# Kernel optimization log

Hardware: AMD Instinct MI355X
Metric: run time of the kernel (lower is better)

The kernel has to match this reference:

```python
import jax, jax.numpy as jnp
import numpy as np
from jax import lax

B, S, L, H, D_IN, W = 128, 64, 137, 128, 64, 256  # batch, segments, logsig_dim, hidden, input_dim, vf_width


def setup_inputs() -> dict:
    key = jax.random.key(0)
    ks = jax.random.split(key, 12)
    rn = lambda k, s, sc: jax.random.normal(k, s, dtype=jnp.float32) * sc
    return {
        "times": jnp.arange(S + 1, dtype=jnp.float32),
        "logsig": rn(ks[0], (B, S, L), 0.1),
        "initial": rn(ks[1], (B, D_IN), 1.0),
        "in_w": rn(ks[2], (D_IN, H), 0.12),
        "in_b": rn(ks[3], (H,), 0.05),
        "h1_w": rn(ks[4], (H, W), 0.09),
        "h1_b": rn(ks[5], (W,), 0.05),
        "h2_w": rn(ks[6], (W, W), 0.06),
        "h2_b": rn(ks[7], (W,), 0.05),
        "vo_w": rn(ks[8], (W, W), 0.06),
        "vo_b": rn(ks[9], (W,), 0.05),
        "ml_w": rn(ks[10], (W, H * (L - 1)), 0.02),
        "ml_b": rn(ks[11], (H * (L - 1),), 0.01),
    }


def reference(times, logsig, initial, in_w, in_b, h1_w, h1_b, h2_w, h2_b, vo_w, vo_b, ml_w, ml_b):
    intervals = times                 # [S+1]; forward requires times == registered intervals
    coeffs = logsig[:, :, 1:]         # [B, S, L-1] (first logsig channel dropped)
    h0 = initial @ in_w + in_b        # [B, H]

    def func(t, y):
        # searchsorted + clamp, exactly as in the torch module
        idx = jnp.clip(jnp.searchsorted(intervals, t, side='left'), 1, S)
        dt = intervals[idx] - intervals[idx - 1]
        coeff = jnp.take(coeffs, idx - 1, axis=1)        # [B, L-1]
        h = jax.nn.relu(y @ h1_w + h1_b)                 # vf MLP (vf_depth-1 = 2 hidden layers)
        h = jax.nn.relu(h @ h2_w + h2_b)
        h = jnp.tanh(h @ vo_w + vo_b)                    # final tanh activation
        vf = (h @ ml_w + ml_b).reshape(B, H, L - 1)      # [B, H, L-1]
        return jnp.einsum('bhd,bd->bh', vf, coeff) / dt  # [B, H]

    def step(y, n):
        # one fixed-size Heun (RK2) step from intervals[n] to intervals[n+1]
        t0, t1 = intervals[n], intervals[n + 1]
        dt = t1 - t0
        k1 = func(t0, y)
        k2 = func(t1, y + dt * k1)
        y1 = y + 0.5 * dt * (k1 + k2)
        return y1, y1

    _, ys = lax.scan(step, h0, jnp.arange(S))            # ys: [S, B, H]
    features = jnp.concatenate([h0[:, None, :], jnp.swapaxes(ys, 0, 1)], axis=1)  # [B, S+1, H]
    return features, features[:, -1]
```

## Files before the change

kernel.cpp:

```cpp
#include <hip/hip_runtime.h>
#include <hip/hip_bf16.h>


#define BB 128
#define SS 64
#define LL 137
#define HH 128
#define DIN 64
#define WW 256
#define DD 136
#define KP 160
#define NC 32768
#define OUT2_OFF ((size_t)BB*(SS+1)*HH)

typedef __hip_bfloat16 bf16;
typedef __attribute__((ext_vector_type(8))) short short8;
typedef __attribute__((ext_vector_type(4))) float f32x4;
typedef _Float16 h2t __attribute__((ext_vector_type(2)));

__device__ __forceinline__ bf16 f2bf(float x){ return __float2bfloat16(x); }

__device__ __forceinline__ float fdot2u(unsigned w, unsigned y, float acc){
#if __has_builtin(__builtin_amdgcn_fdot2)
  return __builtin_amdgcn_fdot2(__builtin_bit_cast(h2t, w),
                                __builtin_bit_cast(h2t, y), acc, false);
#else
  h2t a = __builtin_bit_cast(h2t, w), b2 = __builtin_bit_cast(h2t, y);
  return acc + (float)a[0]*(float)b2[0] + (float)a[1]*(float)b2[1];
#endif
}
__device__ __forceinline__ float dot8(uint4 w, uint4 y, float acc){
  acc = fdot2u(w.x, y.x, acc);
  acc = fdot2u(w.y, y.y, acc);
  acc = fdot2u(w.z, y.z, acc);
  acc = fdot2u(w.w, y.w, acc);
  return acc;
}

__global__ void prep_coeff(const float* __restrict__ logsig, bf16* __restrict__ cA){
  int m = blockIdx.x;
  int d = threadIdx.x;
  int a = m >> 7, b = m & 127;
  float v = 0.0f;
  if (d < DD) v = logsig[(size_t)(b*SS + a)*LL + 1 + d];
  cA[(size_t)m*KP + d] = f2bf(v);
}

__global__ void prep_btt(const float* __restrict__ mlw, bf16* __restrict__ btt){
  int c = blockIdx.x;
  int d = threadIdx.x;
  int w = ((c >> 10) << 3) | (c & 7);
  int h = (c >> 3) & 127;
  float v = 0.0f;
  if (d < DD) v = mlw[(size_t)w*(HH*DD) + h*DD + d];
  btt[(size_t)c*KP + d] = f2bf(v);
}

__global__ void prep_packw(const float* __restrict__ src, uint4* __restrict__ dst){
  int c = blockIdx.x, j = threadIdx.x;
  union { _Float16 h[8]; uint4 v; } u;
  #pragma unroll
  for (int r = 0; r < 8; ++r) u.h[r] = (_Float16)src[(size_t)(c*8+r)*WW + j];
  dst[c*WW + j] = u.v;
}

__global__ void abias_kernel(const float* __restrict__ mlb, const float* __restrict__ logsig,
                             float* __restrict__ Abias){
  int a = blockIdx.x, b = blockIdx.y;
  int h = threadIdx.x;
  __shared__ float cf[DD];
  for (int d = h; d < DD; d += HH) cf[d] = logsig[(size_t)(b*SS + a)*LL + 1 + d];
  __syncthreads();
  float acc = 0.f;
  const float* mb = mlb + (size_t)h*DD;
  #pragma unroll 8
  for (int d = 0; d < DD; ++d) acc += cf[d] * mb[d];
  Abias[((size_t)a*BB + b)*HH + h] = acc;
}

#define AST 40
__global__ __launch_bounds__(256) void agemm_kernel(const bf16* __restrict__ cA,
                                                    const bf16* __restrict__ btt,
                                                    _Float16* __restrict__ As, int mAbs0){
  __shared__ __align__(16) short a_sm[64*AST];
  __shared__ __align__(16) short b_sm[128*AST];
  __shared__ __align__(16) short o_sm[64*136];
  int mt = blockIdx.x, nt = blockIdx.y;
  int t = threadIdx.x, lane = t & 63, wid = t >> 6;
  int mBlockAbs = mAbs0 + mt*64;
  int c0 = nt*128;
  int mW = (wid & 1)*32, cW = (wid >> 1)*64;

  f32x4 acc[2][4];
  for (int i = 0; i < 2; ++i)
    for (int j = 0; j < 4; ++j)
      acc[i][j] = (f32x4){0.f,0.f,0.f,0.f};

  for (int kk = 0; kk < 5; ++kk){
    int d0 = kk*32;
    {
      int row = t >> 2, seg = t & 3;
      uint4 v = *(const uint4*)(cA + (size_t)(mBlockAbs+row)*KP + d0 + seg*8);
      *(uint4*)&a_sm[row*AST + seg*8] = v;
    }
    #pragma unroll
    for (int rep = 0; rep < 2; ++rep){
      int idx = t + rep*256;
      int row = idx >> 2, seg = idx & 3;
      uint4 v = *(const uint4*)(btt + (size_t)(c0+row)*KP + d0 + seg*8);
      *(uint4*)&b_sm[row*AST + seg*8] = v;
    }
    __syncthreads();
    int mr = lane & 15, q = lane >> 4;
    short8 af[2], bfr[4];
    #pragma unroll
    for (int mi = 0; mi < 2; ++mi) af[mi]  = *(const short8*)&a_sm[(mW + mi*16 + mr)*AST + q*8];
    #pragma unroll
    for (int ci = 0; ci < 4; ++ci) bfr[ci] = *(const short8*)&b_sm[(cW + ci*16 + mr)*AST + q*8];
    #pragma unroll
    for (int mi = 0; mi < 2; ++mi)
      #pragma unroll
      for (int ci = 0; ci < 4; ++ci)
        acc[mi][ci] = __builtin_amdgcn_mfma_f32_16x16x32_bf16(af[mi], bfr[ci], acc[mi][ci], 0, 0, 0);
    __syncthreads();
  }

  {
    int mr = lane & 15, q = lane >> 4;
    #pragma unroll
    for (int mi = 0; mi < 2; ++mi)
      #pragma unroll
      for (int ci = 0; ci < 4; ++ci){
        int col = cW + ci*16 + mr;
        #pragma unroll
        for (int r = 0; r < 4; ++r){
          int row = mW + mi*16 + q*4 + r;
          _Float16 hv = (_Float16)acc[mi][ci][r];
          o_sm[row*136 + col] = *(short*)&hv;
        }
      }
  }
  __syncthreads();
  int mLocBlock = mt*64;
  #pragma unroll
  for (int rep = 0; rep < 4; ++rep){
    int idx = t + rep*256;
    int row = idx >> 4, seg = idx & 15;
    uint4 v = *(const uint4*)&o_sm[row*136 + seg*8];
    *(uint4*)(As + (size_t)(mLocBlock + row)*NC + c0 + seg*8) = v;
  }
}

__device__ __forceinline__ void nrde_func(
    int b, int wave, int lane,
    const uint4* __restrict__ wp1, const uint4* __restrict__ wp2,
    const uint4* vo_sm,
    const _Float16* yh, _Float16* h1h, _Float16* h2h, _Float16* h3h,
    const float* bs1, const float* bs2, const float* bsv,
    const _Float16* __restrict__ As, const float* __restrict__ Abias,
    int aLoc, int aAbs, float inv_dtf, float* kout)
{
  const int j = (wave << 4) | (lane & 15);
  const int q = lane >> 4;
  {
    const uint4* wp = wp1 + (q << 2)*WW + j;
    const uint4* yp = (const uint4*)yh + (q << 2);
    float acc = 0.f;
    #pragma unroll
    for (int cc = 0; cc < 4; ++cc) acc = dot8(wp[cc*WW], yp[cc], acc);
    acc += __shfl_xor(acc, 16);
    acc += __shfl_xor(acc, 32);
    if (q == 0){ float v = bs1[j] + acc; h1h[j] = (_Float16)(v > 0.f ? v : 0.f); }
  }
  __syncthreads();
  {
    const uint4* wp = wp2 + (q << 3)*WW + j;
    const uint4* hp = (const uint4*)h1h + (q << 3);
    float acc = 0.f;
    #pragma unroll
    for (int cc = 0; cc < 8; ++cc) acc = dot8(wp[cc*WW], hp[cc], acc);
    acc += __shfl_xor(acc, 16);
    acc += __shfl_xor(acc, 32);
    if (q == 0){ float v = bs2[j] + acc; h2h[j] = (_Float16)(v > 0.f ? v : 0.f); }
  }
  __syncthreads();
  {
    const uint4* wp = vo_sm + (q << 3)*WW + j;
    const uint4* hp = (const uint4*)h2h + (q << 3);
    float acc = 0.f;
    #pragma unroll
    for (int cc = 0; cc < 8; ++cc) acc = dot8(wp[cc*WW], hp[cc], acc);
    acc += __shfl_xor(acc, 16);
    acc += __shfl_xor(acc, 32);
    if (q == 0) h3h[j] = (_Float16)tanhf(bsv[j] + acc);
  }
  __syncthreads();
  {
    const int h  = (wave << 3) | (lane & 7);
    const int q8 = lane >> 3;
    const uint4* Ap = (const uint4*)(As + (size_t)(aLoc*BB + b)*NC);
    const uint4* hp = (const uint4*)h3h + (q8 << 2);
    float ab = (q8 == 0) ? Abias[((size_t)aAbs*BB + b)*HH + h] : 0.f;
    float acc = 0.f;
    #pragma unroll
    for (int cc = 0; cc < 4; ++cc)
      acc = dot8(Ap[((q8 << 2) + cc)*HH + h], hp[cc], acc);
    acc += ab;
    acc += __shfl_xor(acc, 8);
    acc += __shfl_xor(acc, 16);
    acc += __shfl_xor(acc, 32);
    if (q8 == 0) kout[h] = acc * inv_dtf;
  }
}

__global__ __launch_bounds__(1024) void scan_kernel(
    const float* __restrict__ times, const float* __restrict__ initial,
    const float* __restrict__ in_w, const float* __restrict__ in_b,
    const float* __restrict__ h1_b, const float* __restrict__ h2_b,
    const float* __restrict__ vo_b,
    const uint4* __restrict__ wp1, const uint4* __restrict__ wp2,
    const uint4* __restrict__ wpv,
    const _Float16* __restrict__ As, const float* __restrict__ Abias,
    float* __restrict__ y_state, float* __restrict__ out,
    int s0, int s1, int aBase)
{
  __shared__ __align__(16) uint4 vo_sm[32*WW];
  __shared__ __align__(16) _Float16 yh[HH];
  __shared__ __align__(16) _Float16 h1h[WW];
  __shared__ __align__(16) _Float16 h2h[WW];
  __shared__ __align__(16) _Float16 h3h[WW];
  __shared__ float yv[HH], kk1[HH], kk2[HH];
  __shared__ float bs1[WW], bs2[WW], bsv[WW];

  const int b = blockIdx.x, t = threadIdx.x;
  const int wave = t >> 6, lane = t & 63;

  for (int i = t; i < 32*WW; i += 1024) vo_sm[i] = wpv[i];
  if (t < WW){ bs1[t] = h1_b[t]; bs2[t] = h2_b[t]; bsv[t] = vo_b[t]; }

  if (s0 == 0){
    if (t < HH){
      float acc = in_b[t];
      for (int i = 0; i < DIN; ++i)
        acc += initial[b*DIN + i] * in_w[(size_t)i*HH + t];
      yv[t] = acc; yh[t] = (_Float16)acc;
      out[(size_t)b*(SS+1)*HH + t] = acc;
    }
  } else if (t < HH){
    float v = y_state[b*HH + t];
    yv[t] = v; yh[t] = (_Float16)v;
  }
  __syncthreads();

  for (int n = s0; n < s1; ++n){
    float t0v = times[n], t1v = times[n+1];
    float dt = t1v - t0v;
    int idx1 = (n >= 1) ? n : 1;
    float dtf1 = times[idx1] - times[idx1-1];
    int a1 = (n >= 1) ? (n-1) : 0;
    nrde_func(b, wave, lane, wp1, wp2, vo_sm, yh, h1h, h2h, h3h, bs1, bs2, bsv,
              As, Abias, a1 - aBase, a1, 1.f/dtf1, kk1);
    __syncthreads();
    if (t < HH) yh[t] = (_Float16)(yv[t] + dt*kk1[t]);
    __syncthreads();
    nrde_func(b, wave, lane, wp1, wp2, vo_sm, yh, h1h, h2h, h3h, bs1, bs2, bsv,
              As, Abias, n - aBase, n, 1.f/dt, kk2);
    __syncthreads();
    if (t < HH){
      float ynew = yv[t] + 0.5f*dt*(kk1[t] + kk2[t]);
      yv[t] = ynew; yh[t] = (_Float16)ynew;
      out[((size_t)b*(SS+1) + (n+1))*HH + t] = ynew;
    }
    __syncthreads();
  }

  if (t < HH){
    y_state[b*HH + t] = yv[t];
    if (s1 == SS) out[OUT2_OFF + (size_t)b*HH + t] = yv[t];
  }
}

extern "C" void kernel_launch(void* const* d_in, const int* in_sizes, int n_in,
                              void* d_out, int out_size, void* d_ws, size_t ws_size,
                              hipStream_t stream)
{
  (void)in_sizes; (void)n_in; (void)out_size;
  const float* times   = (const float*)d_in[0];
  const float* logsig  = (const float*)d_in[1];
  const float* initial = (const float*)d_in[2];
  const float* in_w    = (const float*)d_in[3];
  const float* in_b    = (const float*)d_in[4];
  const float* h1_w    = (const float*)d_in[5];
  const float* h1_b    = (const float*)d_in[6];
  const float* h2_w    = (const float*)d_in[7];
  const float* h2_b    = (const float*)d_in[8];
  const float* vo_w    = (const float*)d_in[9];
  const float* vo_b    = (const float*)d_in[10];
  const float* ml_w    = (const float*)d_in[11];
  const float* ml_b    = (const float*)d_in[12];
  float* out = (float*)d_out;

  char* ws = (char*)d_ws;
  size_t off = 0;
  bf16* cA      = (bf16*)(ws + off); off += (size_t)8192*KP*2;
  bf16* btt     = (bf16*)(ws + off); off += (size_t)NC*KP*2;
  float* Abias  = (float*)(ws + off); off += (size_t)SS*BB*HH*4;
  float* y_state= (float*)(ws + off); off += (size_t)BB*HH*4;
  uint4* wp1    = (uint4*)(ws + off); off += (size_t)16*WW*16;
  uint4* wp2    = (uint4*)(ws + off); off += (size_t)32*WW*16;
  uint4* wpv    = (uint4*)(ws + off); off += (size_t)32*WW*16;
  _Float16* As  = (_Float16*)(ws + off);
  size_t perA = (size_t)BB*HH*WW*2;
  size_t avail = (ws_size > off) ? (ws_size - off) : 0;
  int C = (int)(avail / perA);
  if (C > SS) C = SS;
  if (C < 2) return;

  prep_coeff<<<8192, 160, 0, stream>>>(logsig, cA);
  prep_btt<<<NC, 160, 0, stream>>>(ml_w, btt);
  abias_kernel<<<dim3(SS, BB), HH, 0, stream>>>(ml_b, logsig, Abias);
  prep_packw<<<16, WW, 0, stream>>>(h1_w, wp1);
  prep_packw<<<32, WW, 0, stream>>>(h2_w, wp2);
  prep_packw<<<32, WW, 0, stream>>>(vo_w, wpv);

  int s = 0, aB = 0;
  while (s < SS){
    int cc = SS - aB; if (cc > C) cc = C;
    agemm_kernel<<<dim3(cc*2, 256), 256, 0, stream>>>(cA, btt, As, aB*BB);
    int sEnd = aB + cc; if (sEnd > SS) sEnd = SS;
    scan_kernel<<<BB, 1024, 0, stream>>>(times, initial, in_w, in_b,
        h1_b, h2_b, vo_b, wp1, wp2, wpv, As, Abias, y_state, out, s, sEnd, aB);
    s = sEnd;
    aB = sEnd - 1;
  }
}
```

Measured before the change: 729.9 us.

## Preload GEMM K-slices, prefetch scan weights into registers, use fast tanh

The agemm kernel now loads all five K-slices of A and B into shared memory up front with one barrier, replacing the per-slice load/sync loop, and reuses that buffer for the output staging. In the scan's vector-field function, the global weights for layers 1 and 2 and the As/Abias operands are loaded into registers at function entry, so their latency overlaps the earlier layers instead of sitting between barriers. Dot-product chains are split into two accumulators for more ILP, and tanhf is replaced with an exp/reciprocal approximation. Register pressure rises and the fast tanh slightly changes numerics.

New measurement: 695.5 us. 1.05x faster.

```diff
diff --git a/kernel.cpp b/kernel.cpp
--- a/kernel.cpp
+++ b/kernel.cpp
@@ -37,6 +37,16 @@
   return acc;
 }
 
+__device__ __forceinline__ float fast_tanh(float x){
+  float e = __expf(2.f*x);
+#if __has_builtin(__builtin_amdgcn_rcpf)
+  float r = __builtin_amdgcn_rcpf(e + 1.f);
+#else
+  float r = 1.f/(e + 1.f);
+#endif
+  return 1.f - 2.f*r;
+}
+
 __global__ void prep_coeff(const float* __restrict__ logsig, bf16* __restrict__ cA){
   int m = blockIdx.x;
   int d = threadIdx.x;
@@ -79,74 +89,82 @@
 }
 
 #define AST 40
-__global__ __launch_bounds__(256) void agemm_kernel(const bf16* __restrict__ cA,
-                                                    const bf16* __restrict__ btt,
-                                                    _Float16* __restrict__ As, int mAbs0){
-  __shared__ __align__(16) short a_sm[64*AST];
-  __shared__ __align__(16) short b_sm[128*AST];
-  __shared__ __align__(16) short o_sm[64*136];
+#define ASM_SZ (5*64*AST)
+#define BSM_SZ (5*128*AST)
+__global__ __launch_bounds__(256, 2) void agemm_kernel(const bf16* __restrict__ cA,
+                                                       const bf16* __restrict__ btt,
+                                                       _Float16* __restrict__ As, int mAbs0){
+  __shared__ __align__(16) short sm[ASM_SZ + BSM_SZ];
+  short* a_sm = sm;
+  short* b_sm = sm + ASM_SZ;
   int mt = blockIdx.x, nt = blockIdx.y;
   int t = threadIdx.x, lane = t & 63, wid = t >> 6;
   int mBlockAbs = mAbs0 + mt*64;
   int c0 = nt*128;
   int mW = (wid & 1)*32, cW = (wid >> 1)*64;
 
+  #pragma unroll
+  for (int r = 0; r < 5; ++r){
+    int idx = t + r*256;
+    int kk = idx >> 8, rem = idx & 255;
+    int row = rem >> 2, seg = rem & 3;
+    uint4 v = *(const uint4*)(cA + (size_t)(mBlockAbs+row)*KP + kk*32 + seg*8);
+    *(uint4*)&a_sm[(kk*64 + row)*AST + seg*8] = v;
+  }
+  #pragma unroll
+  for (int r = 0; r < 10; ++r){
+    int idx = t + r*256;
+    int kk = idx >> 9, rem = idx & 511;
+    int row = rem >> 2, seg = rem & 3;
+    uint4 v = *(const uint4*)(btt + (size_t)(c0+row)*KP + kk*32 + seg*8);
+    *(uint4*)&b_sm[(kk*128 + row)*AST + seg*8] = v;
+  }
+  __syncthreads();
+
   f32x4 acc[2][4];
+  #pragma unroll
   for (int i = 0; i < 2; ++i)
+    #pragma unroll
     for (int j = 0; j < 4; ++j)
       acc[i][j] = (f32x4){0.f,0.f,0.f,0.f};
 
+  int mr = lane & 15, q = lane >> 4;
+  #pragma unroll
   for (int kk = 0; kk < 5; ++kk){
-    int d0 = kk*32;
-    {
-      int row = t >> 2, seg = t & 3;
-      uint4 v = *(const uint4*)(cA + (size_t)(mBlockAbs+row)*KP + d0 + seg*8);
-      *(uint4*)&a_sm[row*AST + seg*8] = v;
-    }
-    #pragma unroll
-    for (int rep = 0; rep < 2; ++rep){
-      int idx = t + rep*256;
-      int row = idx >> 2, seg = idx & 3;
-      uint4 v = *(const uint4*)(btt + (size_t)(c0+row)*KP + d0 + seg*8);
-      *(uint4*)&b_sm[row*AST + seg*8] = v;
-    }
-    __syncthreads();
-    int mr = lane & 15, q = lane >> 4;
     short8 af[2], bfr[4];
     #pragma unroll
-    for (int mi = 0; mi < 2; ++mi) af[mi]  = *(const short8*)&a_sm[(mW + mi*16 + mr)*AST + q*8];
-    #pragma unroll
-    for (int ci = 0; ci < 4; ++ci) bfr[ci] = *(const short8*)&b_sm[(cW + ci*16 + mr)*AST + q*8];
+    for (int mi = 0; mi < 2; ++mi)
+      af[mi]  = *(const short8*)&a_sm[(kk*64 + mW + mi*16 + mr)*AST + q*8];
+    #pragma unroll
+    for (int ci = 0; ci < 4; ++ci)
+      bfr[ci] = *(const short8*)&b_sm[(kk*128 + cW + ci*16 + mr)*AST + q*8];
     #pragma unroll
     for (int mi = 0; mi < 2; ++mi)
       #pragma unroll
       for (int ci = 0; ci < 4; ++ci)
         acc[mi][ci] = __builtin_amdgcn_mfma_f32_16x16x32_bf16(af[mi], bfr[ci], acc[mi][ci], 0, 0, 0);
-    __syncthreads();
-  }
-
-  {
-    int mr = lane & 15, q = lane >> 4;
-    #pragma unroll
-    for (int mi = 0; mi < 2; ++mi)
+  }
+  __syncthreads();
+
+  #pragma unroll
+  for (int mi = 0; mi < 2; ++mi)
+    #pragma unroll
+    for (int ci = 0; ci < 4; ++ci){
+      int col = cW + ci*16 + mr;
       #pragma unroll
-      for (int ci = 0; ci < 4; ++ci){
-        int col = cW + ci*16 + mr;
-        #pragma unroll
-        for (int r = 0; r < 4; ++r){
-          int row = mW + mi*16 + q*4 + r;
-          _Float16 hv = (_Float16)acc[mi][ci][r];
-          o_sm[row*136 + col] = *(short*)&hv;
-        }
+      for (int r = 0; r < 4; ++r){
+        int row = mW + mi*16 + q*4 + r;
+        _Float16 hv = (_Float16)acc[mi][ci][r];
+        sm[row*136 + col] = *(short*)&hv;
       }
-  }
+    }
   __syncthreads();
   int mLocBlock = mt*64;
   #pragma unroll
   for (int rep = 0; rep < 4; ++rep){
     int idx = t + rep*256;
     int row = idx >> 4, seg = idx & 15;
-    uint4 v = *(const uint4*)&o_sm[row*136 + seg*8];
+    uint4 v = *(const uint4*)&sm[row*136 + seg*8];
     *(uint4*)(As + (size_t)(mLocBlock + row)*NC + c0 + seg*8) = v;
   }
 }
@@ -160,25 +178,49 @@
     const _Float16* __restrict__ As, const float* __restrict__ Abias,
     int aLoc, int aAbs, float inv_dtf, float* kout)
 {
-  const int j = (wave << 4) | (lane & 15);
-  const int q = lane >> 4;
+  const int j  = (wave << 4) | (lane & 15);
+  const int q  = lane >> 4;
+  const int h  = (wave << 3) | (lane & 7);
+  const int q8 = lane >> 3;
+
+  uint4 w1r[4], w2r[8], ar[4];
   {
     const uint4* wp = wp1 + (q << 2)*WW + j;
+    #pragma unroll
+    for (int cc = 0; cc < 4; ++cc) w1r[cc] = wp[cc*WW];
+  }
+  {
+    const uint4* wp = wp2 + (q << 3)*WW + j;
+    #pragma unroll
+    for (int cc = 0; cc < 8; ++cc) w2r[cc] = wp[cc*WW];
+  }
+  {
+    const uint4* Ap = (const uint4*)(As + ((size_t)aLoc*BB + b)*NC);
+    #pragma unroll
+    for (int cc = 0; cc < 4; ++cc) ar[cc] = Ap[((q8 << 2) + cc)*HH + h];
+  }
+  float ab = (q8 == 0) ? Abias[((size_t)aAbs*BB + b)*HH + h] : 0.f;
+
+  {
     const uint4* yp = (const uint4*)yh + (q << 2);
-    float acc = 0.f;
-    #pragma unroll
-    for (int cc = 0; cc < 4; ++cc) acc = dot8(wp[cc*WW], yp[cc], acc);
+    float a0 = 0.f, a1 = 0.f;
+    a0 = dot8(w1r[0], yp[0], a0); a1 = dot8(w1r[1], yp[1], a1);
+    a0 = dot8(w1r[2], yp[2], a0); a1 = dot8(w1r[3], yp[3], a1);
+    float acc = a0 + a1;
     acc += __shfl_xor(acc, 16);
     acc += __shfl_xor(acc, 32);
     if (q == 0){ float v = bs1[j] + acc; h1h[j] = (_Float16)(v > 0.f ? v : 0.f); }
   }
   __syncthreads();
   {
-    const uint4* wp = wp2 + (q << 3)*WW + j;
     const uint4* hp = (const uint4*)h1h + (q << 3);
-    float acc = 0.f;
-    #pragma unroll
-    for (int cc = 0; cc < 8; ++cc) acc = dot8(wp[cc*WW], hp[cc], acc);
+    float a0 = 0.f, a1 = 0.f;
+    #pragma unroll
+    for (int cc = 0; cc < 8; cc += 2){
+      a0 = dot8(w2r[cc],   hp[cc],   a0);
+      a1 = dot8(w2r[cc+1], hp[cc+1], a1);
+    }
+    float acc = a0 + a1;
     acc += __shfl_xor(acc, 16);
     acc += __shfl_xor(acc, 32);
     if (q == 0){ float v = bs2[j] + acc; h2h[j] = (_Float16)(v > 0.f ? v : 0.f); }
@@ -187,25 +229,24 @@
   {
     const uint4* wp = vo_sm + (q << 3)*WW + j;
     const uint4* hp = (const uint4*)h2h + (q << 3);
-    float acc = 0.f;
-    #pragma unroll
-    for (int cc = 0; cc < 8; ++cc) acc = dot8(wp[cc*WW], hp[cc], acc);
+    float a0 = 0.f, a1 = 0.f;
+    #pragma unroll
+    for (int cc = 0; cc < 8; cc += 2){
+      a0 = dot8(wp[cc*WW],     hp[cc],   a0);
+      a1 = dot8(wp[(cc+1)*WW], hp[cc+1], a1);
+    }
+    float acc = a0 + a1;
     acc += __shfl_xor(acc, 16);
     acc += __shfl_xor(acc, 32);
-    if (q == 0) h3h[j] = (_Float16)tanhf(bsv[j] + acc);
-  }
-  __syncthreads();
-  {
-    const int h  = (wave << 3) | (lane & 7);
-    const int q8 = lane >> 3;
-    const uint4* Ap = (const uint4*)(As + (size_t)(aLoc*BB + b)*NC);
+    if (q == 0) h3h[j] = (_Float16)fast_tanh(bsv[j] + acc);
+  }
+  __syncthreads();
+  {
     const uint4* hp = (const uint4*)h3h + (q8 << 2);
-    float ab = (q8 == 0) ? Abias[((size_t)aAbs*BB + b)*HH + h] : 0.f;
-    float acc = 0.f;
-    #pragma unroll
-    for (int cc = 0; cc < 4; ++cc)
-      acc = dot8(Ap[((q8 << 2) + cc)*HH + h], hp[cc], acc);
-    acc += ab;
+    float a0 = 0.f, a1 = 0.f;
+    a0 = dot8(ar[0], hp[0], a0); a1 = dot8(ar[1], hp[1], a1);
+    a0 = dot8(ar[2], hp[2], a0); a1 = dot8(ar[3], hp[3], a1);
+    float acc = a0 + a1 + ab;
     acc += __shfl_xor(acc, 8);
     acc += __shfl_xor(acc, 16);
     acc += __shfl_xor(acc, 32);
```
